# Performance work log

Hardware: AMD Instinct MI355X
Metric: run time of the kernel (lower is better)

## Reference

```python
import jax, jax.numpy as jnp
import numpy as np

DIM = 1024
HEADS = 16
DIM_HEAD = 64
INNER = HEADS * DIM_HEAD  # 1024
B, N = 2, 2048


def setup_inputs() -> dict:
    key = jax.random.key(0)
    ks = jax.random.split(key, 6)
    x = jax.random.normal(ks[0], (B, N, DIM), dtype=jnp.float32)
    rel_pos_bias = jax.random.normal(ks[1], (1, HEADS, N, N), dtype=jnp.float32)
    g = jnp.ones((DIM,), dtype=jnp.float32)
    # Linear weights stored torch-style as [out_features, in_features].
    # Note: original zero-inits Wo; we use small random values so outputs/grads are non-trivial.
    Wq = jax.random.normal(ks[2], (INNER, DIM), dtype=jnp.float32) * (DIM ** -0.5)
    Wkv = jax.random.normal(ks[3], (2 * INNER, DIM), dtype=jnp.float32) * (DIM ** -0.5)
    Wo = jax.random.normal(ks[4], (DIM, INNER), dtype=jnp.float32) * (INNER ** -0.5)
    return {"x": x, "rel_pos_bias": rel_pos_bias, "g": g, "Wq": Wq, "Wkv": Wkv, "Wo": Wo}


def reference(x, rel_pos_bias, g, Wq, Wkv, Wo):
    eps = 1e-5  # x is float32
    # Faithful to source: normalize over dim=1 (sequence axis), biased variance.
    mean = jnp.mean(x, axis=1, keepdims=True)          # [b, 1, d]
    var = jnp.var(x, axis=1, keepdims=True)            # [b, 1, d]
    xn = (x - mean) * jax.lax.rsqrt(jnp.maximum(var, eps)) * g

    q = xn @ Wq.T                                      # [b, n, inner]
    kv = xn @ Wkv.T                                    # [b, n, 2*inner]
    k, v = jnp.split(kv, 2, axis=-1)

    def to_heads(t):  # b n (h d) -> b h n d
        b, n, _ = t.shape
        return t.reshape(b, n, HEADS, DIM_HEAD).transpose(0, 2, 1, 3)

    q, k, v = to_heads(q), to_heads(k), to_heads(v)
    q = q * (DIM_HEAD ** -0.5)

    sim = jnp.einsum('bhid,bhjd->bhij', q, k) + rel_pos_bias  # [b, h, n, n]
    attn = jax.nn.softmax(sim, axis=-1)
    out = jnp.einsum('bhij,bhjd->bhid', attn, v)              # [b, h, n, d]
    out = out.transpose(0, 2, 1, 3).reshape(x.shape[0], x.shape[1], INNER)
    return out @ Wo.T                                         # [b, n, dim]
```

## Files before the change

### kernel.cpp

```cpp
#include <hip/hip_runtime.h>
#include <hip/hip_bf16.h>

typedef __bf16 bf16;
typedef __attribute__((ext_vector_type(8))) __bf16 bf16x8;
typedef __attribute__((ext_vector_type(4))) __bf16 bf16x4;
typedef __attribute__((ext_vector_type(4))) float f32x4;
typedef __attribute__((ext_vector_type(16))) float f32x16;
typedef __attribute__((ext_vector_type(4))) unsigned int u32x4;

#define DIMD  1024
#define SEQ   2048
#define BATCH 2
#define HEADS 16
#define INNER 1024
#define QKVN  3072
#define ROWS  (BATCH*SEQ)
#define LOG2E 1.44269504f

__global__ void ln_partial(const float* __restrict__ x,
                           float* __restrict__ psum, float* __restrict__ psq) {
    const int nc = blockIdx.x;
    const int b  = blockIdx.y;
    const int t  = threadIdx.x;
    const float* xp = x + ((size_t)b*SEQ + (size_t)nc*32)*DIMD;
    float s0=0,s1=0,s2=0,s3=0,q0=0,q1=0,q2=0,q3=0;
    for (int r=0; r<32; ++r) {
        const float* row = xp + (size_t)r*DIMD;
        float v0=row[t], v1=row[t+256], v2=row[t+512], v3=row[t+768];
        s0+=v0; q0+=v0*v0; s1+=v1; q1+=v1*v1;
        s2+=v2; q2+=v2*v2; s3+=v3; q3+=v3*v3;
    }
    float* ps = psum + ((size_t)b*64 + nc)*DIMD;
    float* pq = psq  + ((size_t)b*64 + nc)*DIMD;
    ps[t]=s0; ps[t+256]=s1; ps[t+512]=s2; ps[t+768]=s3;
    pq[t]=q0; pq[t+256]=q1; pq[t+512]=q2; pq[t+768]=q3;
}

__global__ void ln_finalize(const float* __restrict__ psum, const float* __restrict__ psq,
                            const float* __restrict__ g,
                            float* __restrict__ scale, float* __restrict__ shift) {
    const int d = blockIdx.x*256 + threadIdx.x;
    const int b = blockIdx.y;
    float s=0.f, q=0.f;
    for (int nc=0; nc<64; ++nc) {
        s += psum[((size_t)b*64+nc)*DIMD + d];
        q += psq [((size_t)b*64+nc)*DIMD + d];
    }
    const float inv_n = 1.f/(float)SEQ;
    float mean = s*inv_n;
    float var  = q*inv_n - mean*mean;
    var = fmaxf(var, 1e-5f);
    scale[b*DIMD+d] = g[d]*rsqrtf(var);
    shift[b*DIMD+d] = mean;
}

__global__ void ln_apply(const float* __restrict__ x,
                         const float* __restrict__ scale, const float* __restrict__ shift,
                         bf16* __restrict__ xn) {
    size_t idx = ((size_t)blockIdx.x*256 + threadIdx.x)*4;
    int b = (int)(idx >> 21);
    int d = (int)(idx & (DIMD-1));
    f32x4 v  = *reinterpret_cast<const f32x4*>(x + idx);
    f32x4 sc = *reinterpret_cast<const f32x4*>(scale + (size_t)b*DIMD + d);
    f32x4 sh = *reinterpret_cast<const f32x4*>(shift + (size_t)b*DIMD + d);
    bf16x4 o;
    o.x = (bf16)((v.x - sh.x)*sc.x);
    o.y = (bf16)((v.y - sh.y)*sc.y);
    o.z = (bf16)((v.z - sh.z)*sc.z);
    o.w = (bf16)((v.w - sh.w)*sc.w);
    *reinterpret_cast<bf16x4*>(xn + idx) = o;
}

__global__ void castk(const float* __restrict__ s, bf16* __restrict__ d, int n, float scl) {
    int i = (blockIdx.x*256 + threadIdx.x)*4;
    if (i >= n) return;
    f32x4 v = *reinterpret_cast<const f32x4*>(s + i);
    bf16x4 o; o.x=(bf16)(v.x*scl); o.y=(bf16)(v.y*scl); o.z=(bf16)(v.z*scl); o.w=(bf16)(v.w*scl);
    *reinterpret_cast<bf16x4*>(d + i) = o;
}

__device__ __forceinline__ void gload16(const void* g, void* l) {
    __builtin_amdgcn_global_load_lds(
        (const __attribute__((address_space(1))) unsigned int*)g,
        (__attribute__((address_space(3))) unsigned int*)l,
        16, 0, 0);
}

__device__ inline void store_out(float* p, float v) { *p = v; }
__device__ inline void store_out(bf16*  p, float v) { *p = (bf16)v; }

template <typename OT>
__global__ __launch_bounds__(256, 2)
void gemm_bt(const bf16* __restrict__ A, const bf16* __restrict__ B,
             OT* __restrict__ C, int M, int N, int K) {
    __shared__ bf16 As[128*64];
    __shared__ bf16 Bs[128*64];
    const int t = threadIdx.x;
    const int wave = t >> 6, lane = t & 63;
    const int wr = wave >> 1, wc = wave & 1;
    const int m0 = blockIdx.y*128, n0 = blockIdx.x*128;
    const int lr = lane & 15, lg = lane >> 4;
    const int srow = wave*32 + (lane>>3);
    const int scol = (lane&7)*8;

    f32x4 acc[4][4];
    #pragma unroll
    for (int i=0;i<4;++i)
        #pragma unroll
        for (int j=0;j<4;++j) acc[i][j] = (f32x4){0.f,0.f,0.f,0.f};

    for (int k0=0; k0<K; k0+=64) {
        #pragma unroll
        for (int i=0;i<4;++i) {
            gload16(A + (size_t)(m0+srow+8*i)*K + k0 + scol, As + (srow+8*i)*64 + scol);
            gload16(B + (size_t)(n0+srow+8*i)*K + k0 + scol, Bs + (srow+8*i)*64 + scol);
        }
        __syncthreads();
        #pragma unroll
        for (int kk=0; kk<2; ++kk) {
            bf16x8 a[4], b[4];
            #pragma unroll
            for (int mi=0;mi<4;++mi)
                a[mi] = *reinterpret_cast<const bf16x8*>(As + (wr*64+mi*16+lr)*64 + kk*32+lg*8);
            #pragma unroll
            for (int ni=0;ni<4;++ni)
                b[ni] = *reinterpret_cast<const bf16x8*>(Bs + (wc*64+ni*16+lr)*64 + kk*32+lg*8);
            #pragma unroll
            for (int mi=0;mi<4;++mi)
                #pragma unroll
                for (int ni=0;ni<4;++ni)
                    acc[mi][ni] = __builtin_amdgcn_mfma_f32_16x16x32_bf16(a[mi], b[ni], acc[mi][ni], 0, 0, 0);
        }
        __syncthreads();
    }
    #pragma unroll
    for (int mi=0;mi<4;++mi)
        #pragma unroll
        for (int ni=0;ni<4;++ni)
            #pragma unroll
            for (int r=0;r<4;++r) {
                int row = m0 + wr*64 + mi*16 + lg*4 + r;
                int col = n0 + wc*64 + ni*16 + lr;
                store_out(&C[(size_t)row*N + col], acc[mi][ni][r]);
            }
}

__global__ __launch_bounds__(256)
void transpose_v(const bf16* __restrict__ qkv, bf16* __restrict__ vT) {
    __shared__ bf16 tile[64][72];
    const int nt = blockIdx.x, h = blockIdx.y, b = blockIdx.z;
    const int t = threadIdx.x;
    const bf16* src = qkv + ((size_t)(b*SEQ + nt*64))*QKVN + 2*INNER + h*64;
    #pragma unroll
    for (int i=0;i<2;++i) {
        int c = t + 256*i, row = c>>3, col = (c&7)*8;
        *reinterpret_cast<bf16x8*>(&tile[row][col]) =
            *reinterpret_cast<const bf16x8*>(src + (size_t)row*QKVN + col);
    }
    __syncthreads();
    bf16* dst = vT + ((size_t)(b*HEADS + h))*64*SEQ + nt*64;
    #pragma unroll
    for (int i=0;i<2;++i) {
        int c = t + 256*i, d = c>>3, n0 = (c&7)*8;
        bf16x8 v;
        #pragma unroll
        for (int j=0;j<8;++j) v[j] = tile[n0+j][d];
        *reinterpret_cast<bf16x8*>(dst + (size_t)d*SEQ + n0) = v;
    }
}


__device__ __forceinline__ unsigned pk2(float a, float b) {
    union { bf16 h[2]; unsigned u; } x;
    x.h[0] = (bf16)a; x.h[1] = (bf16)b;
    return x.u;
}

#define ATTN_BARRIER()                                         \
    __builtin_amdgcn_sched_barrier(0);                         \
    asm volatile("s_waitcnt lgkmcnt(0)" ::: "memory");         \
    __builtin_amdgcn_s_barrier();                              \
    __builtin_amdgcn_sched_barrier(0)

#define ATTN_ITER(CUR, T)                                                          \
  {                                                                                \
                       \
    if ((T)+1 < 32) {                                                              \
      *reinterpret_cast<bf16x8*>(&Ks[0][(CUR)^1][st_off])  = krA;                  \
      *reinterpret_cast<bf16x8*>(&Ks[1][(CUR)^1][st_off])  = krB;                  \
      *reinterpret_cast<bf16x8*>(&VTs[0][(CUR)^1][st_off]) = vrA;                  \
      *reinterpret_cast<bf16x8*>(&VTs[1][(CUR)^1][st_off]) = vrB;                  \
    }                                                                              \
                   \
    if ((T)+2 < 32) {                                                              \
      krA = *reinterpret_cast<const bf16x8*>(kbase0 + (size_t)(((T)+2)*64+srow)*QKVN + scol);  \
      krB = *reinterpret_cast<const bf16x8*>(kbase1 + (size_t)(((T)+2)*64+srow)*QKVN + scol);  \
      vrA = *reinterpret_cast<const bf16x8*>(vtb0 + (size_t)srow*SEQ + ((T)+2)*64 + scol);     \
      vrB = *reinterpret_cast<const bf16x8*>(vtb1 + (size_t)srow*SEQ + ((T)+2)*64 + scol);     \
    }                                                                              \
          \
    if ((T)+1 < 32) {                                                              \
      _Pragma("unroll")                                                            \
      for (int B2=0;B2<2;++B2)                                                     \
        _Pragma("unroll")                                                          \
        for (int rr=0;rr<4;++rr)                                                   \
          breg[(CUR)^1][B2][rr] = *reinterpret_cast<const f32x4*>(                 \
              brow + ((T)+1)*64 + 32*B2 + 8*rr);                                   \
    }                                                                              \
                                    \
    f32x16 p0 = (f32x16)(0.0f), p1 = (f32x16)(0.0f);                               \
    __builtin_amdgcn_s_setprio(1);                                                 \
    _Pragma("unroll")                                                              \
    for (int s=0;s<4;++s) {                                                        \
      bf16x8 kf0 = *reinterpret_cast<const bf16x8*>(&myK[(CUR)*4096 + koff[0][s]]); \
      p0 = __builtin_amdgcn_mfma_f32_32x32x16_bf16(kf0, qf[s], p0, 0,0,0);         \
      bf16x8 kf1 = *reinterpret_cast<const bf16x8*>(&myK[(CUR)*4096 + koff[1][s]]); \
      p1 = __builtin_amdgcn_mfma_f32_32x32x16_bf16(kf1, qf[s], p1, 0,0,0);         \
    }                                                                              \
    __builtin_amdgcn_s_setprio(0);                                                 \
            \
    float v0[16], v1[16];                                                          \
    _Pragma("unroll")                                                              \
    for (int r=0;r<16;++r) {                                                       \
      v0[r] = __builtin_fmaf(breg[CUR][0][r>>2][r&3], LOG2E, p0[r]);               \
      v1[r] = __builtin_fmaf(breg[CUR][1][r>>2][r&3], LOG2E, p1[r]);               \
    }                                                                              \
    float mx[8];                                                                   \
    _Pragma("unroll")                                                              \
    for (int i=0;i<8;++i)                                                          \
      mx[i] = fmaxf(fmaxf(v0[i], v0[i+8]), fmaxf(v1[i], v1[i+8]));                 \
    _Pragma("unroll")                                                              \
    for (int i=0;i<4;++i) mx[i] = fmaxf(mx[i], mx[i+4]);                           \
    float vmax = fmaxf(fmaxf(mx[0],mx[2]), fmaxf(mx[1],mx[3]));                    \
    vmax = fmaxf(vmax, __shfl_xor(vmax, 32));                                      \
    if (!__all(vmax <= m + 11.5f)) {                                               \
      float mnew = fmaxf(m, vmax);                                                 \
      float sc = __builtin_amdgcn_exp2f(m - mnew);                                 \
      m = mnew; l *= sc;                                                           \
      _Pragma("unroll")                                                            \
      for (int r=0;r<16;++r) {                                                     \
        float scr = __shfl(sc, (r&3)+8*(r>>2)+4*hi);                               \
        accO0[r] *= scr; accO1[r] *= scr;                                          \
      }                                                                            \
    }                                                                              \
    float e0[16], e1[16];                                                          \
    _Pragma("unroll")                                                              \
    for (int r=0;r<16;++r) {                                                       \
      e0[r] = __builtin_amdgcn_exp2f(v0[r] - m);                                   \
      e1[r] = __builtin_amdgcn_exp2f(v1[r] - m);                                   \
    }                                                                              \
    float sm[8];                                                                   \
    _Pragma("unroll")                                                              \
    for (int i=0;i<8;++i) sm[i] = (e0[i]+e0[i+8]) + (e1[i]+e1[i+8]);               \
    _Pragma("unroll")                                                              \
    for (int i=0;i<4;++i) sm[i] += sm[i+4];                                        \
    float rsum = (sm[0]+sm[2]) + (sm[1]+sm[3]);                                    \
    rsum += __shfl_xor(rsum, 32);                                                  \
    l += rsum;                                                                     \
           \
    unsigned W0[4][2], W1[4][2];                                                   \
    _Pragma("unroll")                                                              \
    for (int rr=0;rr<4;++rr) {                                                     \
      W0[rr][0] = pk2(e0[4*rr+0], e0[4*rr+1]);                                     \
      W0[rr][1] = pk2(e0[4*rr+2], e0[4*rr+3]);                                     \
      W1[rr][0] = pk2(e1[4*rr+0], e1[4*rr+1]);                                     \
      W1[rr][1] = pk2(e1[4*rr+2], e1[4*rr+3]);                                     \
    }                                                                              \
                               \
    bf16x8 pa[4];                                                                  \
    _Pragma("unroll")                                                              \
    for (int s4=0;s4<4;++s4) {                                                     \
      unsigned u[4];                                                               \
      _Pragma("unroll")                                                            \
      for (int hh=0;hh<2;++hh) {                                                   \
        unsigned a0 = (s4>>1) ? W1[2*(s4&1)  ][hh] : W0[2*(s4&1)  ][hh];           \
        unsigned a1 = (s4>>1) ? W1[2*(s4&1)+1][hh] : W0[2*(s4&1)+1][hh];           \
        unsigned X = hi ? a0 : a1;                                                 \
        unsigned R = (unsigned)__shfl_xor((int)X, 32);                             \
        u[hh]   = hi ? R  : a0;                                                    \
        u[2+hh] = hi ? a1 : R;                                                     \
      }                                                                            \
      u32x4 uv = {u[0], u[1], u[2], u[3]};                                         \
      pa[s4] = __builtin_bit_cast(bf16x8, uv);                                     \
    }                                                                              \
                                                                        \
    __builtin_amdgcn_s_setprio(1);                                                 \
    _Pragma("unroll")                                                              \
    for (int s4=0;s4<4;++s4) {                                                     \
      bf16x8 vfa = *reinterpret_cast<const bf16x8*>(&myV[(CUR)*4096 + voff[0][s4]]); \
      accO0 = __builtin_amdgcn_mfma_f32_32x32x16_bf16(pa[s4], vfa, accO0, 0,0,0);  \
      bf16x8 vfb = *reinterpret_cast<const bf16x8*>(&myV[(CUR)*4096 + voff[1][s4]]); \
      accO1 = __builtin_amdgcn_mfma_f32_32x32x16_bf16(pa[s4], vfb, accO1, 0,0,0);  \
    }                                                                              \
    __builtin_amdgcn_s_setprio(0);                                                 \
    ATTN_BARRIER();                                                                \
  }

__global__ __launch_bounds__(512, 2)
void attn_kernel(const bf16* __restrict__ qkv, const bf16* __restrict__ vTg,
                 const float* __restrict__ bias, bf16* __restrict__ oh) {
    __shared__ bf16 Ks[2][2][64*64];
    __shared__ bf16 VTs[2][2][64*64];

    const int qt = blockIdx.x, h = blockIdx.y;
    const int t = threadIdx.x;
    const int w = t >> 6, lane = t & 63;
    const int wb = w >> 2;
    const int wq = w & 3;
    const int ql = lane & 31, hi = lane >> 5;
    const int q0 = qt*128;

    int koff[2][4], voff[2][4];
    #pragma unroll
    for (int B2=0;B2<2;++B2)
        #pragma unroll
        for (int s=0;s<4;++s) {
            koff[B2][s] = (32*B2+ql)*64 + (((2*s+hi) ^ (ql&7))*8);
            voff[B2][s] = (32*B2+ql)*64 + (((2*s+hi) ^ (ql&7))*8);
        }
    bf16* myK = (bf16*)Ks[wb];
    bf16* myV = (bf16*)VTs[wb];

    const int srow = t>>3;
    const int scol = (t&7)*8;
    const int st_off = srow*64 + (((t&7) ^ (srow&7))*8);

    const bf16* qrow = qkv + ((size_t)(wb*SEQ + q0 + wq*32 + ql))*QKVN + h*64 + hi*8;
    bf16x8 qf[4];
    #pragma unroll
    for (int s=0;s<4;++s)
        qf[s] = *reinterpret_cast<const bf16x8*>(qrow + 16*s);

    const bf16* kbase0 = qkv + INNER + h*64;
    const bf16* kbase1 = qkv + (size_t)SEQ*QKVN + INNER + h*64;
    const bf16* vtb0   = vTg + (size_t)h*64*SEQ;
    const bf16* vtb1   = vTg + (size_t)(HEADS + h)*64*SEQ;
    const float* brow = bias + ((size_t)h*SEQ + (size_t)(q0 + wq*32 + ql))*SEQ + 4*hi;

    bf16x8 krA, krB, vrA, vrB;
    f32x4 breg[2][2][4];

    *reinterpret_cast<bf16x8*>(&Ks[0][0][st_off]) =
        *reinterpret_cast<const bf16x8*>(kbase0 + (size_t)srow*QKVN + scol);
    *reinterpret_cast<bf16x8*>(&Ks[1][0][st_off]) =
        *reinterpret_cast<const bf16x8*>(kbase1 + (size_t)srow*QKVN + scol);
    *reinterpret_cast<bf16x8*>(&VTs[0][0][st_off]) =
        *reinterpret_cast<const bf16x8*>(vtb0 + (size_t)srow*SEQ + scol);
    *reinterpret_cast<bf16x8*>(&VTs[1][0][st_off]) =
        *reinterpret_cast<const bf16x8*>(vtb1 + (size_t)srow*SEQ + scol);
    krA = *reinterpret_cast<const bf16x8*>(kbase0 + (size_t)(64+srow)*QKVN + scol);
    krB = *reinterpret_cast<const bf16x8*>(kbase1 + (size_t)(64+srow)*QKVN + scol);
    vrA = *reinterpret_cast<const bf16x8*>(vtb0 + (size_t)srow*SEQ + 64 + scol);
    vrB = *reinterpret_cast<const bf16x8*>(vtb1 + (size_t)srow*SEQ + 64 + scol);
    #pragma unroll
    for (int B2=0;B2<2;++B2)
        #pragma unroll
        for (int rr=0;rr<4;++rr)
            breg[0][B2][rr] = *reinterpret_cast<const f32x4*>(brow + 32*B2 + 8*rr);
    ATTN_BARRIER();

    float m = -__builtin_inff();
    float l = 0.f;
    f32x16 accO0 = (f32x16)(0.0f), accO1 = (f32x16)(0.0f);

    for (int t2 = 0; t2 < 32; t2 += 2) {
        ATTN_ITER(0, t2);
        ATTN_ITER(1, t2+1);
    }

    float linv = 1.f/l;
    bf16* ob = oh + ((size_t)(wb*SEQ + q0 + wq*32))*INNER + h*64 + ql;
    #pragma unroll
    for (int r=0;r<16;++r) {
        int qoff = (r&3) + 8*(r>>2) + 4*hi;
        float li = __shfl(linv, qoff);
        ob[(size_t)qoff*INNER]      = (bf16)(accO0[r]*li);
        ob[(size_t)qoff*INNER + 32] = (bf16)(accO1[r]*li);
    }
}

extern "C" void kernel_launch(void* const* d_in, const int* in_sizes, int n_in,
                              void* d_out, int out_size, void* d_ws, size_t ws_size,
                              hipStream_t stream) {
    const float* x    = (const float*)d_in[0];
    const float* bias = (const float*)d_in[1];
    const float* g    = (const float*)d_in[2];
    const float* Wq   = (const float*)d_in[3];
    const float* Wkv  = (const float*)d_in[4];
    const float* Wo   = (const float*)d_in[5];
    float* out = (float*)d_out;

    char* ws = (char*)d_ws;
    bf16*  xn    = (bf16*)(ws);
    bf16*  vT    = (bf16*)(ws);
    bf16*  wqkv  = (bf16*)(ws + 8388608);
    bf16*  wo    = (bf16*)(ws + 14680064);
    bf16*  qkv   = (bf16*)(ws + 16777216);
    bf16*  oh    = (bf16*)(ws + 41943040);
    float* psum  = (float*)(ws + 50331648);
    float* psq   = (float*)(ws + 50855936);
    float* scale = (float*)(ws + 51380224);
    float* shift = (float*)(ws + 51388416);

    ln_partial <<<dim3(64,2), 256, 0, stream>>>(x, psum, psq);
    ln_finalize<<<dim3(4,2),  256, 0, stream>>>(psum, psq, g, scale, shift);
    ln_apply   <<<dim3(4096), 256, 0, stream>>>(x, scale, shift, xn);

    castk<<<dim3(1024), 256, 0, stream>>>(Wq,  wqkv,           1048576, 0.125f*LOG2E);
    castk<<<dim3(2048), 256, 0, stream>>>(Wkv, wqkv + 1048576, 2097152, 1.0f);
    castk<<<dim3(1024), 256, 0, stream>>>(Wo,  wo,             1048576, 1.0f);

    gemm_bt<bf16><<<dim3(24,32), 256, 0, stream>>>(xn, wqkv, qkv, ROWS, QKVN, DIMD);

    transpose_v<<<dim3(32,16,2), 256, 0, stream>>>(qkv, vT);

    attn_kernel<<<dim3(16,16), 512, 0, stream>>>(qkv, vT, bias, oh);

    gemm_bt<float><<<dim3(8,32), 256, 0, stream>>>(oh, wo, out, ROWS, INNER, INNER);
}
```

Before: 211.6 us.

## Stage relative-position bias through swizzled LDS with coalesced loads

```diff
diff --git a/kernel.cpp b/kernel.cpp
--- a/kernel.cpp
+++ b/kernel.cpp
@@ -184,28 +184,25 @@
 
 #define ATTN_ITER(CUR, T)                                                          \
   {                                                                                \
-                       \
+              \
     if ((T)+1 < 32) {                                                              \
       *reinterpret_cast<bf16x8*>(&Ks[0][(CUR)^1][st_off])  = krA;                  \
       *reinterpret_cast<bf16x8*>(&Ks[1][(CUR)^1][st_off])  = krB;                  \
       *reinterpret_cast<bf16x8*>(&VTs[0][(CUR)^1][st_off]) = vrA;                  \
       *reinterpret_cast<bf16x8*>(&VTs[1][(CUR)^1][st_off]) = vrB;                  \
-    }                                                                              \
-                   \
+      _Pragma("unroll")                                                            \
+      for (int i=0;i<4;++i)                                                        \
+        *reinterpret_cast<f32x4*>(&BsL[(CUR)^1][bst[i]]) = breg[i];                \
+    }                                                                              \
+                      \
     if ((T)+2 < 32) {                                                              \
       krA = *reinterpret_cast<const bf16x8*>(kbase0 + (size_t)(((T)+2)*64+srow)*QKVN + scol);  \
       krB = *reinterpret_cast<const bf16x8*>(kbase1 + (size_t)(((T)+2)*64+srow)*QKVN + scol);  \
       vrA = *reinterpret_cast<const bf16x8*>(vtb0 + (size_t)srow*SEQ + ((T)+2)*64 + scol);     \
       vrB = *reinterpret_cast<const bf16x8*>(vtb1 + (size_t)srow*SEQ + ((T)+2)*64 + scol);     \
-    }                                                                              \
-          \
-    if ((T)+1 < 32) {                                                              \
       _Pragma("unroll")                                                            \
-      for (int B2=0;B2<2;++B2)                                                     \
-        _Pragma("unroll")                                                          \
-        for (int rr=0;rr<4;++rr)                                                   \
-          breg[(CUR)^1][B2][rr] = *reinterpret_cast<const f32x4*>(                 \
-              brow + ((T)+1)*64 + 32*B2 + 8*rr);                                   \
+      for (int i=0;i<4;++i)                                                        \
+        breg[i] = *reinterpret_cast<const f32x4*>(bgl + (size_t)(32*i)*SEQ + ((T)+2)*64);      \
     }                                                                              \
                                     \
     f32x16 p0 = (f32x16)(0.0f), p1 = (f32x16)(0.0f);                               \
@@ -218,12 +215,19 @@
       p1 = __builtin_amdgcn_mfma_f32_32x32x16_bf16(kf1, qf[s], p1, 0,0,0);         \
     }                                                                              \
     __builtin_amdgcn_s_setprio(0);                                                 \
+                              \
+    f32x4 bb0[4], bb1[4];                                                          \
+    _Pragma("unroll")                                                              \
+    for (int rr=0;rr<4;++rr) {                                                     \
+      bb0[rr] = *reinterpret_cast<const f32x4*>(&BsL[CUR][brd[0][rr]]);            \
+      bb1[rr] = *reinterpret_cast<const f32x4*>(&BsL[CUR][brd[1][rr]]);            \
+    }                                                                              \
             \
     float v0[16], v1[16];                                                          \
     _Pragma("unroll")                                                              \
     for (int r=0;r<16;++r) {                                                       \
-      v0[r] = __builtin_fmaf(breg[CUR][0][r>>2][r&3], LOG2E, p0[r]);               \
-      v1[r] = __builtin_fmaf(breg[CUR][1][r>>2][r&3], LOG2E, p1[r]);               \
+      v0[r] = __builtin_fmaf(bb0[r>>2][r&3], LOG2E, p0[r]);                        \
+      v1[r] = __builtin_fmaf(bb1[r>>2][r&3], LOG2E, p1[r]);                        \
     }                                                                              \
     float mx[8];                                                                   \
     _Pragma("unroll")                                                              \
@@ -296,11 +300,12 @@
     ATTN_BARRIER();                                                                \
   }
 
-__global__ __launch_bounds__(512, 2)
+__global__ __launch_bounds__(512, 1)
 void attn_kernel(const bf16* __restrict__ qkv, const bf16* __restrict__ vTg,
                  const float* __restrict__ bias, bf16* __restrict__ oh) {
     __shared__ bf16 Ks[2][2][64*64];
     __shared__ bf16 VTs[2][2][64*64];
+    __shared__ float BsL[2][128*64];
 
     const int qt = blockIdx.x, h = blockIdx.y;
     const int t = threadIdx.x;
@@ -321,6 +326,21 @@
     bf16* myK = (bf16*)Ks[wb];
     bf16* myV = (bf16*)VTs[wb];
 
+    int bst[4];
+    {
+        int rlow = t>>4;
+        int swg  = ((t&15) ^ (rlow&15))*4;
+        #pragma unroll
+        for (int i=0;i<4;++i)
+            bst[i] = (32*i + rlow)*64 + swg;
+    }
+    int brd[2][4];
+    #pragma unroll
+    for (int B2=0;B2<2;++B2)
+        #pragma unroll
+        for (int rr=0;rr<4;++rr)
+            brd[B2][rr] = (wq*32+ql)*64 + (((8*B2+2*rr+hi) ^ (ql&15))*4);
+
     const int srow = t>>3;
     const int scol = (t&7)*8;
     const int st_off = srow*64 + (((t&7) ^ (srow&7))*8);
@@ -335,10 +355,10 @@
     const bf16* kbase1 = qkv + (size_t)SEQ*QKVN + INNER + h*64;
     const bf16* vtb0   = vTg + (size_t)h*64*SEQ;
     const bf16* vtb1   = vTg + (size_t)(HEADS + h)*64*SEQ;
-    const float* brow = bias + ((size_t)h*SEQ + (size_t)(q0 + wq*32 + ql))*SEQ + 4*hi;
+    const float* bgl = bias + ((size_t)h*SEQ + (size_t)(q0 + (t>>4)))*SEQ + 4*(t&15);
 
     bf16x8 krA, krB, vrA, vrB;
-    f32x4 breg[2][2][4];
+    f32x4 breg[4];
 
     *reinterpret_cast<bf16x8*>(&Ks[0][0][st_off]) =
         *reinterpret_cast<const bf16x8*>(kbase0 + (size_t)srow*QKVN + scol);
@@ -348,15 +368,19 @@
         *reinterpret_cast<const bf16x8*>(vtb0 + (size_t)srow*SEQ + scol);
     *reinterpret_cast<bf16x8*>(&VTs[1][0][st_off]) =
         *reinterpret_cast<const bf16x8*>(vtb1 + (size_t)srow*SEQ + scol);
+    #pragma unroll
+    for (int i=0;i<4;++i)
+        breg[i] = *reinterpret_cast<const f32x4*>(bgl + (size_t)(32*i)*SEQ);
+    #pragma unroll
+    for (int i=0;i<4;++i)
+        *reinterpret_cast<f32x4*>(&BsL[0][bst[i]]) = breg[i];
     krA = *reinterpret_cast<const bf16x8*>(kbase0 + (size_t)(64+srow)*QKVN + scol);
     krB = *reinterpret_cast<const bf16x8*>(kbase1 + (size_t)(64+srow)*QKVN + scol);
     vrA = *reinterpret_cast<const bf16x8*>(vtb0 + (size_t)srow*SEQ + 64 + scol);
     vrB = *reinterpret_cast<const bf16x8*>(vtb1 + (size_t)srow*SEQ + 64 + scol);
     #pragma unroll
-    for (int B2=0;B2<2;++B2)
-        #pragma unroll
-        for (int rr=0;rr<4;++rr)
-            breg[0][B2][rr] = *reinterpret_cast<const f32x4*>(brow + 32*B2 + 8*rr);
+    for (int i=0;i<4;++i)
+        breg[i] = *reinterpret_cast<const f32x4*>(bgl + (size_t)(32*i)*SEQ + 64);
     ATTN_BARRIER();
 
     float m = -__builtin_inff();
```

Result: faster. 181.6 us (-14.2%).

## Stage attention bias via async global-to-LDS triple buffer; merge weight casts

Applied to the files above, without the earlier changes.

```diff
diff --git a/kernel.cpp b/kernel.cpp
--- a/kernel.cpp
+++ b/kernel.cpp
@@ -71,12 +71,19 @@
     *reinterpret_cast<bf16x4*>(xn + idx) = o;
 }
 
-__global__ void castk(const float* __restrict__ s, bf16* __restrict__ d, int n, float scl) {
+__global__ void castk_all(const float* __restrict__ Wq, const float* __restrict__ Wkv,
+                          const float* __restrict__ Wo,
+                          bf16* __restrict__ wqkv, bf16* __restrict__ wo, float qs) {
     int i = (blockIdx.x*256 + threadIdx.x)*4;
-    if (i >= n) return;
-    f32x4 v = *reinterpret_cast<const f32x4*>(s + i);
-    bf16x4 o; o.x=(bf16)(v.x*scl); o.y=(bf16)(v.y*scl); o.z=(bf16)(v.z*scl); o.w=(bf16)(v.w*scl);
-    *reinterpret_cast<bf16x4*>(d + i) = o;
+    f32x4 v; bf16* dst;
+    if (i < 1048576)      { v = *reinterpret_cast<const f32x4*>(Wq + i);
+                            v.x*=qs; v.y*=qs; v.z*=qs; v.w*=qs; dst = wqkv + i; }
+    else if (i < 3145728) { v = *reinterpret_cast<const f32x4*>(Wkv + (i-1048576));
+                            dst = wqkv + i; }
+    else                  { v = *reinterpret_cast<const f32x4*>(Wo + (i-3145728));
+                            dst = wo + (i-3145728); }
+    bf16x4 o; o.x=(bf16)v.x; o.y=(bf16)v.y; o.z=(bf16)v.z; o.w=(bf16)v.w;
+    *reinterpret_cast<bf16x4*>(dst) = o;
 }
 
 __device__ __forceinline__ void gload16(const void* g, void* l) {
@@ -182,31 +189,35 @@
     __builtin_amdgcn_s_barrier();                              \
     __builtin_amdgcn_sched_barrier(0)
 
+#define STAGE_BIAS(BUF, TT)                                                      \
+  {                                                                              \
+    float* bdst_ = BsL + (size_t)(BUF)*8192 + t*4;                               \
+    _Pragma("unroll")                                                            \
+    for (int i_=0;i_<4;++i_)                                                     \
+        gload16(bptr + (size_t)(32*i_)*SEQ + (TT)*64, bdst_ + i_*2048);          \
+  }
+
 #define ATTN_ITER(CUR, T)                                                          \
   {                                                                                \
                        \
+         \
     if ((T)+1 < 32) {                                                              \
       *reinterpret_cast<bf16x8*>(&Ks[0][(CUR)^1][st_off])  = krA;                  \
       *reinterpret_cast<bf16x8*>(&Ks[1][(CUR)^1][st_off])  = krB;                  \
       *reinterpret_cast<bf16x8*>(&VTs[0][(CUR)^1][st_off]) = vrA;                  \
       *reinterpret_cast<bf16x8*>(&VTs[1][(CUR)^1][st_off]) = vrB;                  \
     }                                                                              \
-                   \
+    __builtin_amdgcn_sched_barrier(0);                                             \
+         \
+    if ((T)+2 < 32) STAGE_BIAS(biasWr, (T)+2);                                     \
+    __builtin_amdgcn_sched_barrier(0);                                             \
+                                                \
     if ((T)+2 < 32) {                                                              \
       krA = *reinterpret_cast<const bf16x8*>(kbase0 + (size_t)(((T)+2)*64+srow)*QKVN + scol);  \
       krB = *reinterpret_cast<const bf16x8*>(kbase1 + (size_t)(((T)+2)*64+srow)*QKVN + scol);  \
       vrA = *reinterpret_cast<const bf16x8*>(vtb0 + (size_t)srow*SEQ + ((T)+2)*64 + scol);     \
       vrB = *reinterpret_cast<const bf16x8*>(vtb1 + (size_t)srow*SEQ + ((T)+2)*64 + scol);     \
     }                                                                              \
-          \
-    if ((T)+1 < 32) {                                                              \
-      _Pragma("unroll")                                                            \
-      for (int B2=0;B2<2;++B2)                                                     \
-        _Pragma("unroll")                                                          \
-        for (int rr=0;rr<4;++rr)                                                   \
-          breg[(CUR)^1][B2][rr] = *reinterpret_cast<const f32x4*>(                 \
-              brow + ((T)+1)*64 + 32*B2 + 8*rr);                                   \
-    }                                                                              \
                                     \
     f32x16 p0 = (f32x16)(0.0f), p1 = (f32x16)(0.0f);                               \
     __builtin_amdgcn_s_setprio(1);                                                 \
@@ -218,12 +229,20 @@
       p1 = __builtin_amdgcn_mfma_f32_32x32x16_bf16(kf1, qf[s], p1, 0,0,0);         \
     }                                                                              \
     __builtin_amdgcn_s_setprio(0);                                                 \
+                                \
+    const float* bcur_ = BsL + (size_t)biasRd*8192;                                \
+    f32x4 bb0[4], bb1[4];                                                          \
+    _Pragma("unroll")                                                              \
+    for (int rr=0;rr<4;++rr) {                                                     \
+      bb0[rr] = *reinterpret_cast<const f32x4*>(&bcur_[brd[0][rr]]);               \
+      bb1[rr] = *reinterpret_cast<const f32x4*>(&bcur_[brd[1][rr]]);               \
+    }                                                                              \
             \
     float v0[16], v1[16];                                                          \
     _Pragma("unroll")                                                              \
     for (int r=0;r<16;++r) {                                                       \
-      v0[r] = __builtin_fmaf(breg[CUR][0][r>>2][r&3], LOG2E, p0[r]);               \
-      v1[r] = __builtin_fmaf(breg[CUR][1][r>>2][r&3], LOG2E, p1[r]);               \
+      v0[r] = __builtin_fmaf(bb0[r>>2][r&3], LOG2E, p0[r]);                        \
+      v1[r] = __builtin_fmaf(bb1[r>>2][r&3], LOG2E, p1[r]);                        \
     }                                                                              \
     float mx[8];                                                                   \
     _Pragma("unroll")                                                              \
@@ -294,13 +313,17 @@
     }                                                                              \
     __builtin_amdgcn_s_setprio(0);                                                 \
     ATTN_BARRIER();                                                                \
+    biasRd = (biasRd==2) ? 0 : biasRd+1;                                           \
+    biasWr = (biasWr==2) ? 0 : biasWr+1;                                           \
   }
 
-__global__ __launch_bounds__(512, 2)
+__global__ __launch_bounds__(512, 1)
 void attn_kernel(const bf16* __restrict__ qkv, const bf16* __restrict__ vTg,
                  const float* __restrict__ bias, bf16* __restrict__ oh) {
     __shared__ bf16 Ks[2][2][64*64];
     __shared__ bf16 VTs[2][2][64*64];
+    __shared__ float BsLarr[3*128*64];
+    float* BsL = BsLarr;
 
     const int qt = blockIdx.x, h = blockIdx.y;
     const int t = threadIdx.x;
@@ -321,6 +344,13 @@
     bf16* myK = (bf16*)Ks[wb];
     bf16* myV = (bf16*)VTs[wb];
 
+    int brd[2][4];
+    #pragma unroll
+    for (int B2=0;B2<2;++B2)
+        #pragma unroll
+        for (int rr=0;rr<4;++rr)
+            brd[B2][rr] = (wq*32+ql)*64 + (((8*B2+2*rr+hi) ^ (ql&15))*4);
+
     const int srow = t>>3;
     const int scol = (t&7)*8;
     const int st_off = srow*64 + (((t&7) ^ (srow&7))*8);
@@ -335,11 +365,15 @@
     const bf16* kbase1 = qkv + (size_t)SEQ*QKVN + INNER + h*64;
     const bf16* vtb0   = vTg + (size_t)h*64*SEQ;
     const bf16* vtb1   = vTg + (size_t)(HEADS + h)*64*SEQ;
-    const float* brow = bias + ((size_t)h*SEQ + (size_t)(q0 + wq*32 + ql))*SEQ + 4*hi;
+    const float* bptr = bias + ((size_t)h*SEQ + (size_t)(q0 + (t>>4)))*SEQ
+                              + (((t&15) ^ ((t>>4)&15))*4);
 
     bf16x8 krA, krB, vrA, vrB;
-    f32x4 breg[2][2][4];
-
+    int biasRd = 0, biasWr = 2;
+
+    STAGE_BIAS(0, 0);
+    STAGE_BIAS(1, 1);
+    __builtin_amdgcn_sched_barrier(0);
     *reinterpret_cast<bf16x8*>(&Ks[0][0][st_off]) =
         *reinterpret_cast<const bf16x8*>(kbase0 + (size_t)srow*QKVN + scol);
     *reinterpret_cast<bf16x8*>(&Ks[1][0][st_off]) =
@@ -352,12 +386,10 @@
     krB = *reinterpret_cast<const bf16x8*>(kbase1 + (size_t)(64+srow)*QKVN + scol);
     vrA = *reinterpret_cast<const bf16x8*>(vtb0 + (size_t)srow*SEQ + 64 + scol);
     vrB = *reinterpret_cast<const bf16x8*>(vtb1 + (size_t)srow*SEQ + 64 + scol);
-    #pragma unroll
-    for (int B2=0;B2<2;++B2)
-        #pragma unroll
-        for (int rr=0;rr<4;++rr)
-            breg[0][B2][rr] = *reinterpret_cast<const f32x4*>(brow + 32*B2 + 8*rr);
-    ATTN_BARRIER();
+    __builtin_amdgcn_sched_barrier(0);
+    asm volatile("s_waitcnt vmcnt(0) lgkmcnt(0)" ::: "memory");
+    __builtin_amdgcn_s_barrier();
+    __builtin_amdgcn_sched_barrier(0);
 
     float m = -__builtin_inff();
     float l = 0.f;
@@ -406,9 +438,7 @@
     ln_finalize<<<dim3(4,2),  256, 0, stream>>>(psum, psq, g, scale, shift);
     ln_apply   <<<dim3(4096), 256, 0, stream>>>(x, scale, shift, xn);
 
-    castk<<<dim3(1024), 256, 0, stream>>>(Wq,  wqkv,           1048576, 0.125f*LOG2E);
-    castk<<<dim3(2048), 256, 0, stream>>>(Wkv, wqkv + 1048576, 2097152, 1.0f);
-    castk<<<dim3(1024), 256, 0, stream>>>(Wo,  wo,             1048576, 1.0f);
+    castk_all<<<dim3(4096), 256, 0, stream>>>(Wq, Wkv, Wo, wqkv, wo, 0.125f*LOG2E);
 
     gemm_bt<bf16><<<dim3(24,32), 256, 0, stream>>>(xn, wqkv, qkv, ROWS, QKVN, DIMD);
 
```

After: 186.9 us. 11.6% less time.
